# Kernel optimization log

Hardware: AMD Instinct MI355X
Metric: run time of the kernel (lower is better)

Reference implementation:

```python
import jax, jax.numpy as jnp
import numpy as np

B, S, N, E = 8, 64, 512, 32  # batch, seq_size, node_num, embed_size


def setup_inputs() -> dict:
    key = jax.random.key(0)
    k0, k1, k2, k3, k4 = jax.random.split(key, 5)
    x = jax.random.normal(k0, (B, S, N), dtype=jnp.float32)
    # lin_w: Linear(2*S, E) -> weight (E, 2*S), bias (E,)
    W = jax.random.normal(k1, (E, 2 * S), dtype=jnp.float32) * (1.0 / np.sqrt(2 * S))
    b_w = jax.random.normal(k2, (E,), dtype=jnp.float32) * 0.01
    # lin_a: Linear(E, 1) -> weight (E,), bias scalar
    Wa = jax.random.normal(k3, (E,), dtype=jnp.float32) * (1.0 / np.sqrt(E))
    b_a = jax.random.normal(k4, (), dtype=jnp.float32) * 0.01
    return {"x": x, "W": W, "b_w": b_w, "Wa": Wa, "b_a": b_a}


def reference(x, W, b_w, Wa, b_a):
    # Faithful to MP_GAT.forward in eval mode (dropout = identity).
    # Algebraic decomposition: lin_w(cat(vi, vj)) = vi @ Wi^T + vj @ Wj^T + b,
    # where W = [Wi | Wj] along the input dim -- avoids the O(N^2 * 2S) concat.
    s = W.shape[1] // 2
    v = jnp.transpose(x, (0, 2, 1))          # (B, N, S)
    Wi, Wj = W[:, :s], W[:, s:]              # (E, S) each
    ti = jnp.einsum('bns,es->bne', v, Wi)    # (B, N, E)
    tj = jnp.einsum('bns,es->bne', v, Wj)    # (B, N, E)
    pre = ti[:, :, None, :] + tj[:, None, :, :] + b_w  # (B, N, N, E)
    xw = jnp.where(pre > 0, pre, 0.2 * pre)  # LeakyReLU(0.2)
    e = jnp.einsum('bije,e->bij', xw, Wa) + b_a        # (B, N, N) = lin_a(...).squeeze
    attention = jax.nn.softmax(e, axis=2)
    h = jax.nn.sigmoid(jnp.einsum('bij,bjs->bis', attention, v))  # (B, N, S)
    return jnp.transpose(h, (0, 2, 1)), attention      # (B, S, N), (B, N, N)
```

## Files before the change

kernel.cpp:

```cpp
#include <hip/hip_runtime.h>
#include <math.h>

#define BB 8
#define SS 64
#define NN 512
#define EE 32
#define IT 16

typedef __attribute__((ext_vector_type(8))) short short8v;
typedef __attribute__((ext_vector_type(4))) float f32x4;

__device__ __forceinline__ unsigned short f2bf(float f) {
    union { float f; unsigned u; } v; v.f = f;
    unsigned r = v.u + 0x7fffu + ((v.u >> 16) & 1u);
    return (unsigned short)(r >> 16);
}
__device__ __forceinline__ float bflo(unsigned u) { return __uint_as_float(u << 16); }
__device__ __forceinline__ float bfhi(unsigned u) { return __uint_as_float(u & 0xffff0000u); }
__device__ __forceinline__ unsigned packtr(float lo, float hi) {
    return (__float_as_uint(hi) & 0xffff0000u) | (__float_as_uint(lo) >> 16);
}

__global__ __launch_bounds__(128) void proj_kernel(
    const float* __restrict__ x, const float* __restrict__ W,
    const float* __restrict__ b_w, const float* __restrict__ Wa,
    float* __restrict__ tip, unsigned short* __restrict__ tjb,
    float* __restrict__ cip, float* __restrict__ djp)
{
    __shared__ float sW[SS][65];
    const int t = threadIdx.x;
    const int wg = ((blockIdx.x & 7) << 6) | (blockIdx.x >> 3);
    const int b = wg >> 6;
    const int n0 = (wg & 63) << 3;

#pragma unroll
    for (int r = 0; r < 8; ++r) {
        int idx = r * 512 + t * 4;
        float4 w4 = *(const float4*)(W + idx);
        int e = idx >> 7;
        int sp = idx & 127;
        int eo = ((sp >> 6) << 5) | e;
        int s0 = sp & 63;
        sW[s0 + 0][eo] = w4.x;
        sW[s0 + 1][eo] = w4.y;
        sW[s0 + 2][eo] = w4.z;
        sW[s0 + 3][eo] = w4.w;
    }
    __syncthreads();

    const int eo = t & 63;
    const int ng = t >> 6;
    const float* xb = x + (size_t)b * SS * NN + n0 + (ng << 2);
    float a0 = 0.f, a1 = 0.f, a2 = 0.f, a3 = 0.f;
#pragma unroll 8
    for (int s = 0; s < SS; ++s) {
        float wv = sW[s][eo];
        float4 xv = *(const float4*)(xb + (size_t)s * NN);
        a0 = fmaf(wv, xv.x, a0);
        a1 = fmaf(wv, xv.y, a1);
        a2 = fmaf(wv, xv.z, a2);
        a3 = fmaf(wv, xv.w, a3);
    }
    const int e = eo & 31;
    const bool isI = eo < EE;
    if (isI) {
        float bias = b_w[e];
        a0 += bias; a1 += bias; a2 += bias; a3 += bias;
        *(float4*)(tip + ((size_t)(b * EE + e)) * NN + n0 + (ng << 2)) =
            make_float4(a0, a1, a2, a3);
    } else {
        unsigned u0 = f2bf(a0) | ((unsigned)f2bf(a1) << 16);
        unsigned u1 = f2bf(a2) | ((unsigned)f2bf(a3) << 16);
        *(uint2*)(tjb + ((size_t)(b * EE + e)) * NN + n0 + (ng << 2)) =
            make_uint2(u0, u1);
    }

    float wa = Wa[e];
    float r0 = wa * a0, r1 = wa * a1, r2 = wa * a2, r3 = wa * a3;
#pragma unroll
    for (int off = 1; off <= 16; off <<= 1) {
        r0 += __shfl_xor(r0, off);
        r1 += __shfl_xor(r1, off);
        r2 += __shfl_xor(r2, off);
        r3 += __shfl_xor(r3, off);
    }
    if (eo == 0)
        *(float4*)(cip + (size_t)b * NN + n0 + (ng << 2)) = make_float4(r0, r1, r2, r3);
    if (eo == 32)
        *(float4*)(djp + (size_t)b * NN + n0 + (ng << 2)) = make_float4(r0, r1, r2, r3);
}

__global__ __launch_bounds__(1024, 1) void attn_kernel(
    const float* __restrict__ x,
    const float* __restrict__ tip,
    const unsigned short* __restrict__ tjb,
    const float* __restrict__ cip,
    const float* __restrict__ djp,
    const float* __restrict__ Wa,
    float* __restrict__ out0,
    float* __restrict__ out1)
{
    __shared__ __align__(16) unsigned short stj[EE * NN];
    __shared__ __align__(16) unsigned short prT[IT * 520];
    __shared__ __align__(16) float s_tiT[IT][36];
    __shared__ __align__(16) float hp[4][SS][17];
    __shared__ __align__(16) float red[16][2];

    const int t = threadIdx.x;
    const int wg = ((blockIdx.x & 7) << 5) | (blockIdx.x >> 3);
    const int b = wg >> 5;
    const int i0 = (wg & 31) << 4;
    const int lane = t & 63;
    const int w = t >> 6;

    if (t < 512) {
        int i = t & 15, e = t >> 4;
        s_tiT[i][e] = tip[((size_t)(b * EE + e)) * NN + i0 + i];
    }
    {
        const uint4* src = (const uint4*)(tjb + (size_t)b * EE * NN);
        uint4* dst = (uint4*)stj;
#pragma unroll
        for (int r = 0; r < 2; ++r) dst[r * 1024 + t] = src[r * 1024 + t];
    }
    __syncthreads();

    const int ip = t >> 7;
    const int jc = t & 127;
    const int j0 = jc << 2;
    const int ia = 2 * ip, ib2 = 2 * ip + 1;

    float rti0[EE], rti1[EE];
#pragma unroll
    for (int q = 0; q < 8; ++q) {
        float4 v = *(const float4*)&s_tiT[ia][q << 2];
        rti0[4 * q + 0] = v.x; rti0[4 * q + 1] = v.y;
        rti0[4 * q + 2] = v.z; rti0[4 * q + 3] = v.w;
        float4 u = *(const float4*)&s_tiT[ib2][q << 2];
        rti1[4 * q + 0] = u.x; rti1[4 * q + 1] = u.y;
        rti1[4 * q + 2] = u.z; rti1[4 * q + 3] = u.w;
    }

    float acc0[4], acc1[4];
#pragma unroll
    for (int k = 0; k < 4; ++k) { acc0[k] = 0.f; acc1[k] = 0.f; }

#pragma unroll
    for (int e = 0; e < EE; ++e) {
        uint2 d = *(const uint2*)&stj[e * NN + j0];
        float wa = Wa[e];
        float t0 = rti0[e], t1 = rti1[e];
        float tjf[4];
        tjf[0] = bflo(d.x); tjf[1] = bfhi(d.x);
        tjf[2] = bflo(d.y); tjf[3] = bfhi(d.y);
#pragma unroll
        for (int k = 0; k < 4; ++k) {
            acc0[k] = fmaf(fabsf(t0 + tjf[k]), wa, acc0[k]);
            acc1[k] = fmaf(fabsf(t1 + tjf[k]), wa, acc1[k]);
        }
    }

    float4 dj4 = *(const float4*)(djp + (size_t)b * NN + j0);
    float dj[4] = {dj4.x, dj4.y, dj4.z, dj4.w};
    float c0 = cip[(size_t)b * NN + i0 + ia];
    float c1 = cip[(size_t)b * NN + i0 + ib2];
    float pr0[4], pr1[4];
#pragma unroll
    for (int k = 0; k < 4; ++k) {
        pr0[k] = __expf(fmaf(0.4f, acc0[k], 0.6f * (c0 + dj[k])));
        pr1[k] = __expf(fmaf(0.4f, acc1[k], 0.6f * (c1 + dj[k])));
    }

    {
        uint2 pa, pb;
        pa.x = f2bf(pr0[0]) | ((unsigned)f2bf(pr0[1]) << 16);
        pa.y = f2bf(pr0[2]) | ((unsigned)f2bf(pr0[3]) << 16);
        pb.x = f2bf(pr1[0]) | ((unsigned)f2bf(pr1[1]) << 16);
        pb.y = f2bf(pr1[2]) | ((unsigned)f2bf(pr1[3]) << 16);
        *(uint2*)&prT[ia * 520 + j0]  = pa;
        *(uint2*)&prT[ib2 * 520 + j0] = pb;
    }

    float rs0 = pr0[0] + pr0[1] + pr0[2] + pr0[3];
    float rs1 = pr1[0] + pr1[1] + pr1[2] + pr1[3];
#pragma unroll
    for (int off = 1; off <= 32; off <<= 1) {
        rs0 += __shfl_xor(rs0, off);
        rs1 += __shfl_xor(rs1, off);
    }
    if (lane == 0) { red[w][0] = rs0; red[w][1] = rs1; }
    __syncthreads();

    float inv0 = 1.0f / (red[2 * ip][0] + red[2 * ip + 1][0]);
    float inv1 = 1.0f / (red[2 * ip][1] + red[2 * ip + 1][1]);

    *(float4*)(out1 + ((size_t)(b * NN + i0 + ia)) * NN + j0) =
        make_float4(pr0[0]*inv0, pr0[1]*inv0, pr0[2]*inv0, pr0[3]*inv0);
    *(float4*)(out1 + ((size_t)(b * NN + i0 + ib2)) * NN + j0) =
        make_float4(pr1[0]*inv1, pr1[1]*inv1, pr1[2]*inv1, pr1[3]*inv1);

    {
        const int mt = w & 3;
        const int kq = w >> 2;
        const int lm = lane & 15;
        const int ko = lane >> 4;
        const float* xrow = x + ((size_t)(b * SS + mt * 16 + lm)) * NN;

        f32x4 acc = {0.f, 0.f, 0.f, 0.f};
#pragma unroll
        for (int st = 0; st < 4; ++st) {
            const int j = kq * 128 + st * 32 + ko * 8;
            float4 xa = *(const float4*)(xrow + j);
            float4 xb2 = *(const float4*)(xrow + j + 4);
            union { unsigned u[4]; short8v v; } af;
            af.u[0] = packtr(xa.x, xa.y);
            af.u[1] = packtr(xa.z, xa.w);
            af.u[2] = packtr(xb2.x, xb2.y);
            af.u[3] = packtr(xb2.z, xb2.w);
            short8v bf = *(const short8v*)&prT[lm * 520 + j];
            acc = __builtin_amdgcn_mfma_f32_16x16x32_bf16(af.v, bf, acc, 0, 0, 0);
        }
#pragma unroll
        for (int r = 0; r < 4; ++r) {
            int s = mt * 16 + (lane >> 4) * 4 + r;
            hp[kq][s][lm] = acc[r];
        }
    }
    __syncthreads();

    {
        int i = t & 15, s = t >> 4;
        float inv = 1.0f / (red[2 * (i >> 1)][i & 1] + red[2 * (i >> 1) + 1][i & 1]);
        float h = ((hp[0][s][i] + hp[1][s][i]) + (hp[2][s][i] + hp[3][s][i])) * inv;
        out0[((size_t)(b * SS + s)) * NN + i0 + i] = 1.0f / (1.0f + __expf(-h));
    }
}

extern "C" void kernel_launch(void* const* d_in, const int* in_sizes, int n_in,
                              void* d_out, int out_size, void* d_ws, size_t ws_size,
                              hipStream_t stream) {
    const float* x   = (const float*)d_in[0];
    const float* W   = (const float*)d_in[1];
    const float* b_w = (const float*)d_in[2];
    const float* Wa  = (const float*)d_in[3];

    float* out0 = (float*)d_out;
    float* out1 = (float*)d_out + (size_t)BB * SS * NN;

    float* tip = (float*)d_ws;
    unsigned short* tjb = (unsigned short*)(tip + (size_t)BB * EE * NN);
    float* cip = (float*)(tjb + (size_t)BB * EE * NN);
    float* djp = cip + (size_t)BB * NN;

    proj_kernel<<<BB * (NN / 8), 128, 0, stream>>>(x, W, b_w, Wa, tip, tjb, cip, djp);
    attn_kernel<<<BB * (NN / IT), 1024, 0, stream>>>(x, tip, tjb, cip, djp, Wa, out0, out1);
}
```

Baseline: 20.52 us.

## Halve rows per attention block, read ti from global, allow two blocks per CU

Each attention workgroup now handles 8 query rows instead of 16, so twice as many workgroups are launched, and each thread computes 2 columns instead of 4. The shared ti tile and its register copies are removed; ti values are loaded from global memory inside the e-loop. Launch bounds now request two blocks per CU to raise occupancy. The trade-off is more global loads of ti, half of each MFMA tile being wasted on duplicated rows, and the tj shared tile being loaded twice as often overall.

```diff
diff --git a/kernel.cpp b/kernel.cpp
--- a/kernel.cpp
+++ b/kernel.cpp
@@ -5,7 +5,7 @@
 #define SS 64
 #define NN 512
 #define EE 32
-#define IT 16
+#define IT 8
 
 typedef __attribute__((ext_vector_type(8))) short short8v;
 typedef __attribute__((ext_vector_type(4))) float f32x4;
@@ -90,7 +90,7 @@
         *(float4*)(djp + (size_t)b * NN + n0 + (ng << 2)) = make_float4(r0, r1, r2, r3);
 }
 
-__global__ __launch_bounds__(1024, 1) void attn_kernel(
+__global__ __launch_bounds__(1024, 2) void attn_kernel(
     const float* __restrict__ x,
     const float* __restrict__ tip,
     const unsigned short* __restrict__ tjb,
@@ -102,21 +102,16 @@
 {
     __shared__ __align__(16) unsigned short stj[EE * NN];
     __shared__ __align__(16) unsigned short prT[IT * 520];
-    __shared__ __align__(16) float s_tiT[IT][36];
-    __shared__ __align__(16) float hp[4][SS][17];
+    __shared__ __align__(16) float hp[4][SS][12];
     __shared__ __align__(16) float red[16][2];
 
     const int t = threadIdx.x;
-    const int wg = ((blockIdx.x & 7) << 5) | (blockIdx.x >> 3);
-    const int b = wg >> 5;
-    const int i0 = (wg & 31) << 4;
+    const int wg = ((blockIdx.x & 7) << 6) | (blockIdx.x >> 3);
+    const int b = wg >> 6;
+    const int i0 = (wg & 63) << 3;
     const int lane = t & 63;
     const int w = t >> 6;
 
-    if (t < 512) {
-        int i = t & 15, e = t >> 4;
-        s_tiT[i][e] = tip[((size_t)(b * EE + e)) * NN + i0 + i];
-    }
     {
         const uint4* src = (const uint4*)(tjb + (size_t)b * EE * NN);
         uint4* dst = (uint4*)stj;
@@ -125,64 +120,44 @@
     }
     __syncthreads();
 
-    const int ip = t >> 7;
-    const int jc = t & 127;
-    const int j0 = jc << 2;
+    const int ip = __builtin_amdgcn_readfirstlane(threadIdx.x >> 8);
+    const int jc = t & 255;
+    const int j0 = jc << 1;
     const int ia = 2 * ip, ib2 = 2 * ip + 1;
 
-    float rti0[EE], rti1[EE];
-#pragma unroll
-    for (int q = 0; q < 8; ++q) {
-        float4 v = *(const float4*)&s_tiT[ia][q << 2];
-        rti0[4 * q + 0] = v.x; rti0[4 * q + 1] = v.y;
-        rti0[4 * q + 2] = v.z; rti0[4 * q + 3] = v.w;
-        float4 u = *(const float4*)&s_tiT[ib2][q << 2];
-        rti1[4 * q + 0] = u.x; rti1[4 * q + 1] = u.y;
-        rti1[4 * q + 2] = u.z; rti1[4 * q + 3] = u.w;
-    }
-
-    float acc0[4], acc1[4];
-#pragma unroll
-    for (int k = 0; k < 4; ++k) { acc0[k] = 0.f; acc1[k] = 0.f; }
-
-#pragma unroll
+    const float* tia = tip + (size_t)b * EE * NN + i0 + ia;
+    const float* tib = tip + (size_t)b * EE * NN + i0 + ib2;
+
+    float acc0[2], acc1[2];
+    acc0[0] = acc0[1] = acc1[0] = acc1[1] = 0.f;
+
+#pragma unroll 8
     for (int e = 0; e < EE; ++e) {
-        uint2 d = *(const uint2*)&stj[e * NN + j0];
+        unsigned d = *(const unsigned*)&stj[e * NN + j0];
         float wa = Wa[e];
-        float t0 = rti0[e], t1 = rti1[e];
-        float tjf[4];
-        tjf[0] = bflo(d.x); tjf[1] = bfhi(d.x);
-        tjf[2] = bflo(d.y); tjf[3] = bfhi(d.y);
-#pragma unroll
-        for (int k = 0; k < 4; ++k) {
-            acc0[k] = fmaf(fabsf(t0 + tjf[k]), wa, acc0[k]);
-            acc1[k] = fmaf(fabsf(t1 + tjf[k]), wa, acc1[k]);
-        }
-    }
-
-    float4 dj4 = *(const float4*)(djp + (size_t)b * NN + j0);
-    float dj[4] = {dj4.x, dj4.y, dj4.z, dj4.w};
+        float t0 = tia[(size_t)e * NN];
+        float t1 = tib[(size_t)e * NN];
+        float f0 = bflo(d), f1 = bfhi(d);
+        acc0[0] = fmaf(fabsf(t0 + f0), wa, acc0[0]);
+        acc0[1] = fmaf(fabsf(t0 + f1), wa, acc0[1]);
+        acc1[0] = fmaf(fabsf(t1 + f0), wa, acc1[0]);
+        acc1[1] = fmaf(fabsf(t1 + f1), wa, acc1[1]);
+    }
+
+    float2 dj2 = *(const float2*)(djp + (size_t)b * NN + j0);
     float c0 = cip[(size_t)b * NN + i0 + ia];
     float c1 = cip[(size_t)b * NN + i0 + ib2];
-    float pr0[4], pr1[4];
-#pragma unroll
-    for (int k = 0; k < 4; ++k) {
-        pr0[k] = __expf(fmaf(0.4f, acc0[k], 0.6f * (c0 + dj[k])));
-        pr1[k] = __expf(fmaf(0.4f, acc1[k], 0.6f * (c1 + dj[k])));
-    }
-
-    {
-        uint2 pa, pb;
-        pa.x = f2bf(pr0[0]) | ((unsigned)f2bf(pr0[1]) << 16);
-        pa.y = f2bf(pr0[2]) | ((unsigned)f2bf(pr0[3]) << 16);
-        pb.x = f2bf(pr1[0]) | ((unsigned)f2bf(pr1[1]) << 16);
-        pb.y = f2bf(pr1[2]) | ((unsigned)f2bf(pr1[3]) << 16);
-        *(uint2*)&prT[ia * 520 + j0]  = pa;
-        *(uint2*)&prT[ib2 * 520 + j0] = pb;
-    }
-
-    float rs0 = pr0[0] + pr0[1] + pr0[2] + pr0[3];
-    float rs1 = pr1[0] + pr1[1] + pr1[2] + pr1[3];
+    float pr0[2], pr1[2];
+    pr0[0] = __expf(fmaf(0.4f, acc0[0], 0.6f * (c0 + dj2.x)));
+    pr0[1] = __expf(fmaf(0.4f, acc0[1], 0.6f * (c0 + dj2.y)));
+    pr1[0] = __expf(fmaf(0.4f, acc1[0], 0.6f * (c1 + dj2.x)));
+    pr1[1] = __expf(fmaf(0.4f, acc1[1], 0.6f * (c1 + dj2.y)));
+
+    *(unsigned*)&prT[ia * 520 + j0]  = f2bf(pr0[0]) | ((unsigned)f2bf(pr0[1]) << 16);
+    *(unsigned*)&prT[ib2 * 520 + j0] = f2bf(pr1[0]) | ((unsigned)f2bf(pr1[1]) << 16);
+
+    float rs0 = pr0[0] + pr0[1];
+    float rs1 = pr1[0] + pr1[1];
 #pragma unroll
     for (int off = 1; off <= 32; off <<= 1) {
         rs0 += __shfl_xor(rs0, off);
@@ -191,13 +166,15 @@
     if (lane == 0) { red[w][0] = rs0; red[w][1] = rs1; }
     __syncthreads();
 
-    float inv0 = 1.0f / (red[2 * ip][0] + red[2 * ip + 1][0]);
-    float inv1 = 1.0f / (red[2 * ip][1] + red[2 * ip + 1][1]);
-
-    *(float4*)(out1 + ((size_t)(b * NN + i0 + ia)) * NN + j0) =
-        make_float4(pr0[0]*inv0, pr0[1]*inv0, pr0[2]*inv0, pr0[3]*inv0);
-    *(float4*)(out1 + ((size_t)(b * NN + i0 + ib2)) * NN + j0) =
-        make_float4(pr1[0]*inv1, pr1[1]*inv1, pr1[2]*inv1, pr1[3]*inv1);
+    float inv0 = 1.0f / (((red[4*ip][0] + red[4*ip+1][0]) +
+                          (red[4*ip+2][0] + red[4*ip+3][0])));
+    float inv1 = 1.0f / (((red[4*ip][1] + red[4*ip+1][1]) +
+                          (red[4*ip+2][1] + red[4*ip+3][1])));
+
+    *(float2*)(out1 + ((size_t)(b * NN + i0 + ia)) * NN + j0) =
+        make_float2(pr0[0] * inv0, pr0[1] * inv0);
+    *(float2*)(out1 + ((size_t)(b * NN + i0 + ib2)) * NN + j0) =
+        make_float2(pr1[0] * inv1, pr1[1] * inv1);
 
     {
         const int mt = w & 3;
@@ -217,20 +194,23 @@
             af.u[1] = packtr(xa.z, xa.w);
             af.u[2] = packtr(xb2.x, xb2.y);
             af.u[3] = packtr(xb2.z, xb2.w);
-            short8v bf = *(const short8v*)&prT[lm * 520 + j];
+            short8v bf = *(const short8v*)&prT[(lm & 7) * 520 + j];
             acc = __builtin_amdgcn_mfma_f32_16x16x32_bf16(af.v, bf, acc, 0, 0, 0);
         }
-#pragma unroll
-        for (int r = 0; r < 4; ++r) {
-            int s = mt * 16 + (lane >> 4) * 4 + r;
-            hp[kq][s][lm] = acc[r];
+        if (lm < 8) {
+#pragma unroll
+            for (int r = 0; r < 4; ++r) {
+                int s = mt * 16 + (lane >> 4) * 4 + r;
+                hp[kq][s][lm] = acc[r];
+            }
         }
     }
     __syncthreads();
 
-    {
-        int i = t & 15, s = t >> 4;
-        float inv = 1.0f / (red[2 * (i >> 1)][i & 1] + red[2 * (i >> 1) + 1][i & 1]);
+    if (t < 512) {
+        int i = t & 7, s = t >> 3;
+        float inv = 1.0f / (((red[4*(i>>1)][i&1]   + red[4*(i>>1)+1][i&1]) +
+                             (red[4*(i>>1)+2][i&1] + red[4*(i>>1)+3][i&1])));
         float h = ((hp[0][s][i] + hp[1][s][i]) + (hp[2][s][i] + hp[3][s][i])) * inv;
         out0[((size_t)(b * SS + s)) * NN + i0 + i] = 1.0f / (1.0f + __expf(-h));
     }
```

Result: slower. 24.58 us (+19.8%).

## Split fused attention kernel into score and PV kernels with bf16 workspace

Applied to the files above, without the earlier changes.

Replaces the single 1024-thread attention kernel (one block per 16 query rows, loading the whole tj table into shared memory) with two kernels. A score kernel computes unnormalized exp scores over 16x128 tiles, writes them as bf16 to a workspace and records partial row sums. A PV kernel then normalizes, writes the attention output and runs the MFMA product per half of the sequence. This raises block count and occupancy at the cost of an extra launch and a global round trip of the bf16 probability matrix. The normalized attention output is now computed from bf16-rounded probabilities (the old kernel used the fp32 values), and the row sums are taken from those rounded values.

```diff
diff --git a/kernel.cpp b/kernel.cpp
--- a/kernel.cpp
+++ b/kernel.cpp
@@ -5,7 +5,6 @@
 #define SS 64
 #define NN 512
 #define EE 32
-#define IT 16
 
 typedef __attribute__((ext_vector_type(8))) short short8v;
 typedef __attribute__((ext_vector_type(4))) float f32x4;
@@ -90,126 +89,147 @@
         *(float4*)(djp + (size_t)b * NN + n0 + (ng << 2)) = make_float4(r0, r1, r2, r3);
 }
 
-__global__ __launch_bounds__(1024, 1) void attn_kernel(
-    const float* __restrict__ x,
+__global__ __launch_bounds__(256) void score_kernel(
+    const unsigned short* __restrict__ tjb,
     const float* __restrict__ tip,
-    const unsigned short* __restrict__ tjb,
     const float* __restrict__ cip,
     const float* __restrict__ djp,
     const float* __restrict__ Wa,
+    unsigned short* __restrict__ prws,
+    float* __restrict__ psum)
+{
+    __shared__ __align__(16) unsigned short stj[EE * 128];
+    __shared__ __align__(16) float s_ti[EE][16];
+
+    const int t = threadIdx.x;
+    const int bid = blockIdx.x;
+    const int b = bid & 7;
+    const int r = bid >> 3;
+    const int it = r >> 2;
+    const int q = r & 3;
+    const int i0 = it << 4;
+    const int jq = q << 7;
+
+#pragma unroll
+    for (int rr = 0; rr < 2; ++rr) {
+        int idx = t + rr * 256;
+        int e = idx >> 4;
+        int jo = (idx & 15) << 3;
+        *(uint4*)&stj[e * 128 + jo] =
+            *(const uint4*)(tjb + ((size_t)(b * EE + e)) * NN + jq + jo);
+    }
+#pragma unroll
+    for (int rr = 0; rr < 2; ++rr) {
+        int idx = t + rr * 256;
+        int e = idx >> 4, i = idx & 15;
+        s_ti[e][i] = tip[((size_t)(b * EE + e)) * NN + i0 + i];
+    }
+    __syncthreads();
+
+    const int w = t >> 6;
+    const int lanej = t & 63;
+    const int j0 = lanej << 1;
+
+    float acc[4][2];
+#pragma unroll
+    for (int ii = 0; ii < 4; ++ii) { acc[ii][0] = 0.f; acc[ii][1] = 0.f; }
+
+#pragma unroll
+    for (int e = 0; e < EE; ++e) {
+        unsigned d = *(const unsigned*)&stj[e * 128 + j0];
+        float4 tiv = *(const float4*)&s_ti[e][w << 2];
+        float wa = Wa[e];
+        float f0 = bflo(d), f1 = bfhi(d);
+        acc[0][0] = fmaf(fabsf(tiv.x + f0), wa, acc[0][0]);
+        acc[0][1] = fmaf(fabsf(tiv.x + f1), wa, acc[0][1]);
+        acc[1][0] = fmaf(fabsf(tiv.y + f0), wa, acc[1][0]);
+        acc[1][1] = fmaf(fabsf(tiv.y + f1), wa, acc[1][1]);
+        acc[2][0] = fmaf(fabsf(tiv.z + f0), wa, acc[2][0]);
+        acc[2][1] = fmaf(fabsf(tiv.z + f1), wa, acc[2][1]);
+        acc[3][0] = fmaf(fabsf(tiv.w + f0), wa, acc[3][0]);
+        acc[3][1] = fmaf(fabsf(tiv.w + f1), wa, acc[3][1]);
+    }
+
+    float2 dj2 = *(const float2*)(djp + (size_t)b * NN + jq + j0);
+    float rs[4];
+#pragma unroll
+    for (int ii = 0; ii < 4; ++ii) {
+        float ci = cip[(size_t)b * NN + i0 + (w << 2) + ii];
+        float p0 = __expf(fmaf(0.4f, acc[ii][0], 0.6f * (ci + dj2.x)));
+        float p1 = __expf(fmaf(0.4f, acc[ii][1], 0.6f * (ci + dj2.y)));
+        unsigned u = f2bf(p0) | ((unsigned)f2bf(p1) << 16);
+        *(unsigned*)&prws[((size_t)(b * NN + i0 + (w << 2) + ii)) * NN + jq + j0] = u;
+        rs[ii] = bflo(u) + bfhi(u);
+    }
+
+#pragma unroll
+    for (int off = 1; off <= 32; off <<= 1) {
+#pragma unroll
+        for (int ii = 0; ii < 4; ++ii) rs[ii] += __shfl_xor(rs[ii], off);
+    }
+    if (lanej == 0) {
+        *(float4*)&psum[(((size_t)(b * 32 + it)) * 4 + q) * 16 + (w << 2)] =
+            make_float4(rs[0], rs[1], rs[2], rs[3]);
+    }
+}
+
+__global__ __launch_bounds__(512, 2) void pv_kernel(
+    const float* __restrict__ x,
+    const unsigned short* __restrict__ prws,
+    const float* __restrict__ psum,
     float* __restrict__ out0,
     float* __restrict__ out1)
 {
-    __shared__ __align__(16) unsigned short stj[EE * NN];
-    __shared__ __align__(16) unsigned short prT[IT * 520];
-    __shared__ __align__(16) float s_tiT[IT][36];
-    __shared__ __align__(16) float hp[4][SS][17];
-    __shared__ __align__(16) float red[16][2];
+    __shared__ __align__(16) unsigned short prT[16 * 520];
+    __shared__ __align__(16) float hp[4][32][17];
+    __shared__ float s_inv[16];
 
     const int t = threadIdx.x;
-    const int wg = ((blockIdx.x & 7) << 5) | (blockIdx.x >> 3);
-    const int b = wg >> 5;
-    const int i0 = (wg & 31) << 4;
+    const int bid = blockIdx.x;
+    const int b = bid & 7;
+    const int r = bid >> 3;
+    const int it = r >> 1;
+    const int hf = r & 1;
+    const int i0 = it << 4;
     const int lane = t & 63;
     const int w = t >> 6;
 
-    if (t < 512) {
-        int i = t & 15, e = t >> 4;
-        s_tiT[i][e] = tip[((size_t)(b * EE + e)) * NN + i0 + i];
-    }
-    {
-        const uint4* src = (const uint4*)(tjb + (size_t)b * EE * NN);
-        uint4* dst = (uint4*)stj;
-#pragma unroll
-        for (int r = 0; r < 2; ++r) dst[r * 1024 + t] = src[r * 1024 + t];
-    }
-    __syncthreads();
-
-    const int ip = t >> 7;
-    const int jc = t & 127;
-    const int j0 = jc << 2;
-    const int ia = 2 * ip, ib2 = 2 * ip + 1;
-
-    float rti0[EE], rti1[EE];
-#pragma unroll
-    for (int q = 0; q < 8; ++q) {
-        float4 v = *(const float4*)&s_tiT[ia][q << 2];
-        rti0[4 * q + 0] = v.x; rti0[4 * q + 1] = v.y;
-        rti0[4 * q + 2] = v.z; rti0[4 * q + 3] = v.w;
-        float4 u = *(const float4*)&s_tiT[ib2][q << 2];
-        rti1[4 * q + 0] = u.x; rti1[4 * q + 1] = u.y;
-        rti1[4 * q + 2] = u.z; rti1[4 * q + 3] = u.w;
-    }
-
-    float acc0[4], acc1[4];
-#pragma unroll
-    for (int k = 0; k < 4; ++k) { acc0[k] = 0.f; acc1[k] = 0.f; }
-
-#pragma unroll
-    for (int e = 0; e < EE; ++e) {
-        uint2 d = *(const uint2*)&stj[e * NN + j0];
-        float wa = Wa[e];
-        float t0 = rti0[e], t1 = rti1[e];
-        float tjf[4];
-        tjf[0] = bflo(d.x); tjf[1] = bfhi(d.x);
-        tjf[2] = bflo(d.y); tjf[3] = bfhi(d.y);
-#pragma unroll
-        for (int k = 0; k < 4; ++k) {
-            acc0[k] = fmaf(fabsf(t0 + tjf[k]), wa, acc0[k]);
-            acc1[k] = fmaf(fabsf(t1 + tjf[k]), wa, acc1[k]);
-        }
-    }
-
-    float4 dj4 = *(const float4*)(djp + (size_t)b * NN + j0);
-    float dj[4] = {dj4.x, dj4.y, dj4.z, dj4.w};
-    float c0 = cip[(size_t)b * NN + i0 + ia];
-    float c1 = cip[(size_t)b * NN + i0 + ib2];
-    float pr0[4], pr1[4];
-#pragma unroll
-    for (int k = 0; k < 4; ++k) {
-        pr0[k] = __expf(fmaf(0.4f, acc0[k], 0.6f * (c0 + dj[k])));
-        pr1[k] = __expf(fmaf(0.4f, acc1[k], 0.6f * (c1 + dj[k])));
-    }
-
-    {
-        uint2 pa, pb;
-        pa.x = f2bf(pr0[0]) | ((unsigned)f2bf(pr0[1]) << 16);
-        pa.y = f2bf(pr0[2]) | ((unsigned)f2bf(pr0[3]) << 16);
-        pb.x = f2bf(pr1[0]) | ((unsigned)f2bf(pr1[1]) << 16);
-        pb.y = f2bf(pr1[2]) | ((unsigned)f2bf(pr1[3]) << 16);
-        *(uint2*)&prT[ia * 520 + j0]  = pa;
-        *(uint2*)&prT[ib2 * 520 + j0] = pb;
-    }
-
-    float rs0 = pr0[0] + pr0[1] + pr0[2] + pr0[3];
-    float rs1 = pr1[0] + pr1[1] + pr1[2] + pr1[3];
-#pragma unroll
-    for (int off = 1; off <= 32; off <<= 1) {
-        rs0 += __shfl_xor(rs0, off);
-        rs1 += __shfl_xor(rs1, off);
-    }
-    if (lane == 0) { red[w][0] = rs0; red[w][1] = rs1; }
-    __syncthreads();
-
-    float inv0 = 1.0f / (red[2 * ip][0] + red[2 * ip + 1][0]);
-    float inv1 = 1.0f / (red[2 * ip][1] + red[2 * ip + 1][1]);
-
-    *(float4*)(out1 + ((size_t)(b * NN + i0 + ia)) * NN + j0) =
-        make_float4(pr0[0]*inv0, pr0[1]*inv0, pr0[2]*inv0, pr0[3]*inv0);
-    *(float4*)(out1 + ((size_t)(b * NN + i0 + ib2)) * NN + j0) =
-        make_float4(pr1[0]*inv1, pr1[1]*inv1, pr1[2]*inv1, pr1[3]*inv1);
-
-    {
-        const int mt = w & 3;
-        const int kq = w >> 2;
+    {
+        int i = t >> 5, jseg = (t & 31) << 4;
+        const uint4* src = (const uint4*)(prws + ((size_t)(b * NN + i0 + i)) * NN + jseg);
+        uint4* dst = (uint4*)&prT[i * 520 + jseg];
+        dst[0] = src[0];
+        dst[1] = src[1];
+    }
+    if (t < 16) {
+        const float* ps = psum + ((size_t)(b * 32 + it)) * 4 * 16 + t;
+        float S = ps[0] + ps[16] + ps[32] + ps[48];
+        s_inv[t] = 1.0f / S;
+    }
+    __syncthreads();
+
+    {
+        int i = t >> 5, jj = (hf << 8) + ((t & 31) << 3);
+        float inv = s_inv[i];
+        uint4 d = *(const uint4*)&prT[i * 520 + jj];
+        float* dst = out1 + ((size_t)(b * NN + i0 + i)) * NN + jj;
+        *(float4*)(dst)     = make_float4(bflo(d.x)*inv, bfhi(d.x)*inv,
+                                          bflo(d.y)*inv, bfhi(d.y)*inv);
+        *(float4*)(dst + 4) = make_float4(bflo(d.z)*inv, bfhi(d.z)*inv,
+                                          bflo(d.w)*inv, bfhi(d.w)*inv);
+    }
+
+    {
+        const int mt = w & 1;
+        const int kq = w >> 1;
         const int lm = lane & 15;
         const int ko = lane >> 4;
-        const float* xrow = x + ((size_t)(b * SS + mt * 16 + lm)) * NN;
+        const float* xrow = x + ((size_t)(b * SS + (hf << 5) + (mt << 4) + lm)) * NN;
 
         f32x4 acc = {0.f, 0.f, 0.f, 0.f};
 #pragma unroll
         for (int st = 0; st < 4; ++st) {
-            const int j = kq * 128 + st * 32 + ko * 8;
+            const int j = (kq << 7) + (st << 5) + (ko << 3);
             float4 xa = *(const float4*)(xrow + j);
             float4 xb2 = *(const float4*)(xrow + j + 4);
             union { unsigned u[4]; short8v v; } af;
@@ -221,18 +241,18 @@
             acc = __builtin_amdgcn_mfma_f32_16x16x32_bf16(af.v, bf, acc, 0, 0, 0);
         }
 #pragma unroll
-        for (int r = 0; r < 4; ++r) {
-            int s = mt * 16 + (lane >> 4) * 4 + r;
-            hp[kq][s][lm] = acc[r];
+        for (int rr = 0; rr < 4; ++rr) {
+            int s = (mt << 4) + (lane >> 4) * 4 + rr;
+            hp[kq][s][lm] = acc[rr];
         }
     }
     __syncthreads();
 
     {
         int i = t & 15, s = t >> 4;
-        float inv = 1.0f / (red[2 * (i >> 1)][i & 1] + red[2 * (i >> 1) + 1][i & 1]);
-        float h = ((hp[0][s][i] + hp[1][s][i]) + (hp[2][s][i] + hp[3][s][i])) * inv;
-        out0[((size_t)(b * SS + s)) * NN + i0 + i] = 1.0f / (1.0f + __expf(-h));
+        float h = ((hp[0][s][i] + hp[1][s][i]) + (hp[2][s][i] + hp[3][s][i])) * s_inv[i];
+        out0[((size_t)(b * SS + (hf << 5) + s)) * NN + i0 + i] =
+            1.0f / (1.0f + __expf(-h));
     }
 }
 
@@ -251,7 +271,10 @@
     unsigned short* tjb = (unsigned short*)(tip + (size_t)BB * EE * NN);
     float* cip = (float*)(tjb + (size_t)BB * EE * NN);
     float* djp = cip + (size_t)BB * NN;
+    unsigned short* prws = (unsigned short*)(djp + (size_t)BB * NN);
+    float* psum = (float*)(prws + (size_t)BB * NN * NN);
 
     proj_kernel<<<BB * (NN / 8), 128, 0, stream>>>(x, W, b_w, Wa, tip, tjb, cip, djp);
-    attn_kernel<<<BB * (NN / IT), 1024, 0, stream>>>(x, tip, tjb, cip, djp, Wa, out0, out1);
-}
+    score_kernel<<<BB * 32 * 4, 256, 0, stream>>>(tjb, tip, cip, djp, Wa, prws, psum);
+    pv_kernel<<<BB * 32 * 2, 512, 0, stream>>>(x, prws, psum, out0, out1);
+}
```

Result: slower. 22.65 us (+10.4%).
